# Kernel optimization log

Measured on AMD Instinct MI355X. Metric: run time of the kernel, lower is better.

The kernel has to match this reference:

```python
import jax, jax.numpy as jnp
import numpy as np

N_NODES = 10000
N_EDGES = 320000
N_GRAPHS = 64
L = 3  # num_layers


def _gru(a, h, wih, whh, bih, bhh):
    # torch.nn.GRUCell math: input a, hidden h
    gi = a @ wih.T + bih
    gh = h @ whh.T + bhh
    ir, iz, inn = jnp.split(gi, 3, axis=-1)
    hr, hz, hn = jnp.split(gh, 3, axis=-1)
    r = jax.nn.sigmoid(ir + hr)
    z = jax.nn.sigmoid(iz + hz)
    n = jnp.tanh(inn + r * hn)
    return (1.0 - z) * n + z * h


def _ggc(x, src, dst, w, wih, whh, bih, bhh):
    # PyG GatedGraphConv: pad features up to out_channels, then L rounds of
    # (linear -> scatter-add over edges -> GRUCell update)
    out_ch = w.shape[-1]
    if x.shape[-1] < out_ch:
        x = jnp.concatenate(
            [x, jnp.zeros((x.shape[0], out_ch - x.shape[-1]), x.dtype)], axis=-1)
    for i in range(w.shape[0]):
        m = x @ w[i]                                        # [N, C]
        a = jax.ops.segment_sum(m[src], dst, num_segments=N_NODES)  # scatter-add
        x = _gru(a, x, wih, whh, bih, bhh)
    return x


def setup_inputs() -> dict:
    key = jax.random.key(0)
    ks = jax.random.split(key, 16)
    d1, d2 = 128, 256
    s1, s2 = 1.0 / np.sqrt(d1), 1.0 / np.sqrt(d2)
    x = jax.random.normal(ks[0], (N_NODES, d1), dtype=jnp.float32)
    edge_index = jax.random.randint(ks[1], (2, N_EDGES), 0, N_NODES, dtype=jnp.int64)
    batch = jnp.sort(jax.random.randint(ks[2], (N_NODES,), 0, N_GRAPHS, dtype=jnp.int64))
    return {
        "x": x,
        "edge_index": edge_index,
        "batch": batch,
        "w1": jax.random.normal(ks[3], (L, d1, d1), jnp.float32) * s1,
        "gru1_wih": jax.random.normal(ks[4], (3 * d1, d1), jnp.float32) * s1,
        "gru1_whh": jax.random.normal(ks[5], (3 * d1, d1), jnp.float32) * s1,
        "gru1_bih": jax.random.normal(ks[6], (3 * d1,), jnp.float32) * s1,
        "gru1_bhh": jax.random.normal(ks[7], (3 * d1,), jnp.float32) * s1,
        "w2": jax.random.normal(ks[8], (L, d2, d2), jnp.float32) * s2,
        "gru2_wih": jax.random.normal(ks[9], (3 * d2, d2), jnp.float32) * s2,
        "gru2_whh": jax.random.normal(ks[10], (3 * d2, d2), jnp.float32) * s2,
        "gru2_bih": jax.random.normal(ks[11], (3 * d2,), jnp.float32) * s2,
        "gru2_bhh": jax.random.normal(ks[12], (3 * d2,), jnp.float32) * s2,
        "fc_w": jax.random.normal(ks[13], (6, d2), jnp.float32) * s2,
        "fc_b": jnp.zeros((6,), jnp.float32),
    }


def reference(x, edge_index, batch, w1, gru1_wih, gru1_whh, gru1_bih, gru1_bhh,
              w2, gru2_wih, gru2_whh, gru2_bih, gru2_bhh, fc_w, fc_b):
    src, dst = edge_index[0], edge_index[1]
    y = jax.nn.relu(_ggc(x, src, dst, w1, gru1_wih, gru1_whh, gru1_bih, gru1_bhh))
    y = _ggc(y, src, dst, w2, gru2_wih, gru2_whh, gru2_bih, gru2_bhh)
    y = jax.ops.segment_max(y, batch, num_segments=N_GRAPHS)  # global max pool [G, 256]
    return y @ fc_w.T + fc_b  # [G, 6]
```

## Files before the change

### kernel.cpp

```cpp
#include <hip/hip_runtime.h>

#define NN 10000
#define NNP 10112
#define NE 320000
#define NG 64
#define D1 128
#define D2 256
#define MT 158

typedef unsigned short u16;
typedef short v8s __attribute__((ext_vector_type(8)));
typedef float v4f __attribute__((ext_vector_type(4)));

__device__ __forceinline__ u16 f2bf(float x) {
    unsigned u = __float_as_uint(x);
    return (u16)((u + 0x7fffu + ((u >> 16) & 1u)) >> 16);
}
__device__ __forceinline__ float bf2f(u16 b) {
    return __uint_as_float(((unsigned)b) << 16);
}
__device__ __forceinline__ float sigm(float x) { return 1.f / (1.f + __expf(-x)); }
__device__ __forceinline__ float tanh_f(float x) {
    float cx = fminf(fmaxf(x, -15.f), 15.f);
    float e = __expf(2.f * cx);
    return (e - 1.f) / (e + 1.f);
}

#define MF(d, a, b) d = __builtin_amdgcn_mfma_f32_16x16x32_bf16(a, b, d, 0, 0, 0)

#define SWZ(bx, by)                              \
    const int bid_ = blockIdx.x;                 \
    const int l_ = bid_ >> 3;                    \
    const int by = (bid_ & 7) * 20 + l_ % 20;    \
    const int bx = l_ / 20;                      \
    if (by >= MT) return;


__global__ __launch_bounds__(256)
void mm_k(const u16* __restrict__ Ah, const u16* __restrict__ Al,
          const u16* __restrict__ Bh, const u16* __restrict__ Bl,
          float* __restrict__ Cm, int K) {
    SWZ(bx, by)
    const int tid = threadIdx.x;
    const int wave = tid >> 6, lane = tid & 63;
    const int wm = (wave >> 1) * 32, wn = (wave & 1) * 32;
    const int bm = by * 64, bn = bx * 64;
    const int quad = lane >> 4, r16 = lane & 15;
    const int NK = K >> 5;
    const size_t arow = (size_t)(bm >> 6) * (K >> 3);
    const size_t brow = (size_t)(bn >> 6) * (K >> 3);
    const int aoff0 = (wm + r16) * 8;
    const int boff0 = (wn + r16) * 8;

    auto LOAD = [&](int ks, v8s* af, v8s* alf, v8s* bf, v8s* blf) {
        const size_t ach = (arow + (size_t)(ks << 2) + quad) * 512;
        const size_t bch = (brow + (size_t)(ks << 2) + quad) * 512;
#pragma unroll
        for (int i = 0; i < 2; ++i) {
            af[i]  = *(const v8s*)(Ah + ach + aoff0 + i * 128);
            alf[i] = *(const v8s*)(Al + ach + aoff0 + i * 128);
            bf[i]  = *(const v8s*)(Bh + bch + boff0 + i * 128);
            blf[i] = *(const v8s*)(Bl + bch + boff0 + i * 128);
        }
    };

    v4f acc[2][2] = {};
    auto STEP = [&](v8s* af, v8s* alf, v8s* bf, v8s* blf) {
#pragma unroll
        for (int i = 0; i < 2; ++i)
#pragma unroll
            for (int j = 0; j < 2; ++j) {
                MF(acc[i][j], af[i], bf[j]);
                MF(acc[i][j], af[i], blf[j]);
                MF(acc[i][j], alf[i], bf[j]);
            }
    };

    v8s aA[2], lA[2], bA[2], cA[2];
    v8s aB[2], lB[2], bB[2], cB[2];
    LOAD(0, aA, lA, bA, cA);
    for (int ks = 0; ks < NK; ks += 2) {
        LOAD(ks + 1, aB, lB, bB, cB);
        STEP(aA, lA, bA, cA);
        if (ks + 2 < NK) LOAD(ks + 2, aA, lA, bA, cA);
        STEP(aB, lB, bB, cB);
    }

#pragma unroll
    for (int i = 0; i < 2; ++i) {
        int gr0 = bm + wm + i * 16 + quad * 4;
#pragma unroll
        for (int j = 0; j < 2; ++j) {
            int gc = bn + wn + j * 16 + r16;
#pragma unroll
            for (int r = 0; r < 4; ++r) {
                int gr = gr0 + r;
                if (gr < NN) Cm[(size_t)gr * K + gc] = acc[i][j][r];
            }
        }
    }
}

template<int MODE, int OS>
__global__ __launch_bounds__(256)
void giqru_k(const u16* __restrict__ Ah, const u16* __restrict__ Al,
             const u16* __restrict__ Xh, const u16* __restrict__ Xl,
             const u16* __restrict__ WcH, const u16* __restrict__ WcL,
             const float* __restrict__ bih, const float* __restrict__ bhh,
             u16* __restrict__ xh_out, u16* __restrict__ xl_out,
             const int* __restrict__ batch, unsigned* __restrict__ pool,
             int C) {
    SWZ(bx, by)
    const int tid = threadIdx.x;
    const int wave = tid >> 6, lane = tid & 63;
    const int wm = (wave >> 1) * 32, wn = (wave & 1) * 64;
    const int bm = by * 64, bn = bx * 128;
    const int quad = lane >> 4, r16 = lane & 15;
    const int K2 = 2 * C;
    const int NK = K2 >> 5;
    const int CCH = C >> 3;
    const size_t arow = (size_t)(bm >> 6) * CCH;
    const size_t wrow = (size_t)(bn >> 7) * (K2 >> 3);
    const int aoff0 = (wm + r16) * 8;
    const int woff0 = (wn + r16) * 8;

    auto LOAD = [&](int ks, v8s* fah, v8s* fal, v8s* wh, v8s* wl) {
        const int k0 = ks << 5;
        const bool ap = k0 < C;
        const u16* sh = ap ? Ah : Xh;
        const u16* sl = ap ? Al : Xl;
        const int kk = ap ? k0 : k0 - C;
        const size_t ach = (arow + (kk >> 3) + quad) * 512;
        const size_t wch = (wrow + (k0 >> 3) + quad) * 1024;
        const int g2 = ap ? 2 : 3;
#pragma unroll
        for (int i = 0; i < 2; ++i) {
            fah[i] = *(const v8s*)(sh + ach + aoff0 + i * 128);
            fal[i] = *(const v8s*)(sl + ach + aoff0 + i * 128);
        }
        wh[0] = *(const v8s*)(WcH + wch + woff0);
        wl[0] = *(const v8s*)(WcL + wch + woff0);
        wh[1] = *(const v8s*)(WcH + wch + woff0 + 128);
        wl[1] = *(const v8s*)(WcL + wch + woff0 + 128);
        wh[2] = *(const v8s*)(WcH + wch + woff0 + g2 * 128);
        wl[2] = *(const v8s*)(WcL + wch + woff0 + g2 * 128);
    };

    v4f acc[2][4] = {};
    auto STEP = [&](v8s* fah, v8s* fal, v8s* wh, v8s* wl, bool ap) {
#pragma unroll
        for (int i = 0; i < 2; ++i) {
            MF(acc[i][0], fah[i], wh[0]); MF(acc[i][0], fah[i], wl[0]); MF(acc[i][0], fal[i], wh[0]);
            MF(acc[i][1], fah[i], wh[1]); MF(acc[i][1], fah[i], wl[1]); MF(acc[i][1], fal[i], wh[1]);
            if (ap) {
                MF(acc[i][2], fah[i], wh[2]); MF(acc[i][2], fah[i], wl[2]); MF(acc[i][2], fal[i], wh[2]);
            } else {
                MF(acc[i][3], fah[i], wh[2]); MF(acc[i][3], fah[i], wl[2]); MF(acc[i][3], fal[i], wh[2]);
            }
        }
    };

    v8s ahA[2], alA[2], whA[3], wlA[3];
    v8s ahB[2], alB[2], whB[3], wlB[3];
    LOAD(0, ahA, alA, whA, wlA);
    for (int ks = 0; ks < NK; ks += 2) {
        LOAD(ks + 1, ahB, alB, whB, wlB);
        STEP(ahA, alA, whA, wlA, (ks << 5) < C);
        if (ks + 2 < NK) LOAD(ks + 2, ahA, alA, whA, wlA);
        STEP(ahB, alB, whB, wlB, ((ks + 1) << 5) < C);
    }

    const int c = bx * 32 + (wn ? 16 : 0) + r16;
    const float br = bih[c] + bhh[c];
    const float bz = bih[C + c] + bhh[C + c];
    const float bi_n = bih[2 * C + c];
    const float bh_n = bhh[2 * C + c];
    const int cch = c >> 3, cr = c & 7;
#pragma unroll
    for (int i = 0; i < 2; ++i) {
        int R0 = bm + wm + i * 16 + quad * 4;
#pragma unroll
        for (int r = 0; r < 4; ++r) {
            int R = R0 + r;
            if (R >= NN) continue;
            float rr = sigm(acc[i][0][r] + br);
            float zz = sigm(acc[i][1][r] + bz);
            float nn_ = tanh_f(acc[i][2][r] + bi_n + rr * (acc[i][3][r] + bh_n));
            size_t hx = ((size_t)(R >> 6) * CCH + cch) * 512 + ((R & 63) << 3) + cr;
            float h = bf2f(Xh[hx]) + bf2f(Xl[hx]);
            float o = (1.f - zz) * nn_ + zz * h;
            if (MODE == 2) {
                unsigned b = __float_as_uint(o);
                unsigned u = (b & 0x80000000u) ? ~b : (b | 0x80000000u);
                atomicMax(&pool[batch[R] * 256 + c], u);
            } else {
                if (MODE == 1) o = fmaxf(o, 0.f);
                size_t ox = ((size_t)(R >> 6) * (OS >> 3) + cch) * 512 + ((R & 63) << 3) + cr;
                u16 hh = f2bf(o);
                xh_out[ox] = hh;
                xl_out[ox] = f2bf(o - bf2f(hh));
            }
        }
    }
}

__global__ void count_k(const int* __restrict__ dst, int* __restrict__ cnt) {
    int e = blockIdx.x * blockDim.x + threadIdx.x;
    if (e < NE) atomicAdd(&cnt[dst[e]], 1);
}

__global__ void scan_k(const int* __restrict__ cnt, int* __restrict__ off,
                       int* __restrict__ cur) {
    __shared__ int ps[1024];
    const int tid = threadIdx.x;
    const int CH = (NN + 1023) / 1024;
    const int base = tid * CH;
    int s = 0;
    for (int i = 0; i < CH; ++i) {
        int idx = base + i;
        if (idx < NN) s += cnt[idx];
    }
    ps[tid] = s;
    __syncthreads();
    for (int d = 1; d < 1024; d <<= 1) {
        int v = (tid >= d) ? ps[tid - d] : 0;
        __syncthreads();
        ps[tid] += v;
        __syncthreads();
    }
    int run = (tid > 0) ? ps[tid - 1] : 0;
    for (int i = 0; i < CH; ++i) {
        int idx = base + i;
        if (idx <= NN) { off[idx] = run; if (idx < NN) cur[idx] = run; }
        if (idx < NN) run += cnt[idx];
    }
}

__global__ void fill_k(const int* __restrict__ src, const int* __restrict__ dst,
                       int* __restrict__ cur, int* __restrict__ elist) {
    int e = blockIdx.x * blockDim.x + threadIdx.x;
    if (e >= NE) return;
    int p = atomicAdd(&cur[dst[e]], 1);
    elist[p] = src[e];
}

template<int C>
__global__ void gather_k(const float* __restrict__ m, const int* __restrict__ off,
                         const int* __restrict__ elist,
                         u16* __restrict__ ah, u16* __restrict__ al) {
    constexpr int LPN = C / 4;
    const int GB = gridDim.x;
    const int q = GB >> 3, r = GB & 7;
    const int xx = blockIdx.x & 7, oo = blockIdx.x >> 3;
    const int wg = (xx < r ? xx * (q + 1) : r * (q + 1) + (xx - r) * q) + oo;
    int t = wg * 256 + threadIdx.x;
    int node = t / LPN;
    if (node >= NN) return;
    int c = (t % LPN) * 4;
    int s0 = off[node], s1 = off[node + 1];
    v4f a0 = 0.f, a1 = 0.f, a2 = 0.f, a3 = 0.f;
    int i = s0;
    for (; i + 4 <= s1; i += 4) {
        int e0 = elist[i], e1 = elist[i + 1], e2 = elist[i + 2], e3 = elist[i + 3];
        v4f v0 = *(const v4f*)(m + (size_t)e0 * C + c);
        v4f v1 = *(const v4f*)(m + (size_t)e1 * C + c);
        v4f v2 = *(const v4f*)(m + (size_t)e2 * C + c);
        v4f v3 = *(const v4f*)(m + (size_t)e3 * C + c);
        a0 += v0; a1 += v1; a2 += v2; a3 += v3;
    }
    for (; i < s1; ++i) {
        int e = elist[i];
        a0 += *(const v4f*)(m + (size_t)e * C + c);
    }
    v4f acc = (a0 + a1) + (a2 + a3);
    ushort4 h, l;
    h.x = f2bf(acc[0]); l.x = f2bf(acc[0] - bf2f(h.x));
    h.y = f2bf(acc[1]); l.y = f2bf(acc[1] - bf2f(h.y));
    h.z = f2bf(acc[2]); l.z = f2bf(acc[2] - bf2f(h.z));
    h.w = f2bf(acc[3]); l.w = f2bf(acc[3] - bf2f(h.w));
    size_t ox = ((size_t)(node >> 6) * (C >> 3) + (c >> 3)) * 512 + ((node & 63) << 3) + (c & 7);
    *(ushort4*)(ah + ox) = h;
    *(ushort4*)(al + ox) = l;
}

__global__ void prep_k(const float* __restrict__ w1, const float* __restrict__ w2,
                       const float* __restrict__ wih1, const float* __restrict__ whh1,
                       const float* __restrict__ wih2, const float* __restrict__ whh2,
                       const float* __restrict__ xin,
                       u16* __restrict__ B1h, u16* __restrict__ B1l,
                       u16* __restrict__ B2h, u16* __restrict__ B2l,
                       u16* __restrict__ Wc1h, u16* __restrict__ Wc1l,
                       u16* __restrict__ Wc2h, u16* __restrict__ Wc2l,
                       u16* __restrict__ xh, u16* __restrict__ xl) {
    const int n1 = 3 * D1 * D1;
    const int n2 = 3 * D2 * D2;
    const int c1 = 4 * D1 * 2 * D1;
    const int c2 = 4 * D2 * 2 * D2;
    int t = blockIdx.x * blockDim.x + threadIdx.x;
    if (t < n1) {
        int l = t / (D1 * D1), rem = t - l * (D1 * D1);
        int k = rem / D1, n = rem - k * D1;
        float v = w1[t]; u16 h = f2bf(v);
        size_t o = l * D1 * D1 + ((size_t)(n >> 6) * (D1 >> 3) + (k >> 3)) * 512 + ((n & 63) << 3) + (k & 7);
        B1h[o] = h; B1l[o] = f2bf(v - bf2f(h)); return;
    }
    t -= n1;
    if (t < n2) {
        int l = t / (D2 * D2), rem = t - l * (D2 * D2);
        int k = rem / D2, n = rem - k * D2;
        float v = w2[t]; u16 h = f2bf(v);
        size_t o = l * D2 * D2 + ((size_t)(n >> 6) * (D2 >> 3) + (k >> 3)) * 512 + ((n & 63) << 3) + (k & 7);
        B2h[o] = h; B2l[o] = f2bf(v - bf2f(h)); return;
    }
    t -= n2;
    if (t < c1) {
        int jp = t >> 8, k = t & 255;
        int c = ((jp >> 6) << 4) | (jp & 15);
        int g = (jp >> 4) & 3;
        float v;
        if (g == 0)      v = (k < D1) ? wih1[c * D1 + k]            : whh1[c * D1 + k - D1];
        else if (g == 1) v = (k < D1) ? wih1[(D1 + c) * D1 + k]     : whh1[(D1 + c) * D1 + k - D1];
        else if (g == 2) v = (k < D1) ? wih1[(2 * D1 + c) * D1 + k] : 0.f;
        else             v = (k < D1) ? 0.f : whh1[(2 * D1 + c) * D1 + k - D1];
        u16 h = f2bf(v);
        size_t o = ((size_t)(jp >> 7) * 32 + (k >> 3)) * 1024 + ((jp & 127) << 3) + (k & 7);
        Wc1h[o] = h; Wc1l[o] = f2bf(v - bf2f(h)); return;
    }
    t -= c1;
    if (t < c2) {
        int jp = t >> 9, k = t & 511;
        int c = ((jp >> 6) << 4) | (jp & 15);
        int g = (jp >> 4) & 3;
        float v;
        if (g == 0)      v = (k < D2) ? wih2[c * D2 + k]            : whh2[c * D2 + k - D2];
        else if (g == 1) v = (k < D2) ? wih2[(D2 + c) * D2 + k]     : whh2[(D2 + c) * D2 + k - D2];
        else if (g == 2) v = (k < D2) ? wih2[(2 * D2 + c) * D2 + k] : 0.f;
        else             v = (k < D2) ? 0.f : whh2[(2 * D2 + c) * D2 + k - D2];
        u16 h = f2bf(v);
        size_t o = ((size_t)(jp >> 7) * 64 + (k >> 3)) * 1024 + ((jp & 127) << 3) + (k & 7);
        Wc2h[o] = h; Wc2l[o] = f2bf(v - bf2f(h)); return;
    }
    t -= c2;
    if (t < NN * D1) {
        int n = t >> 7, cc = t & 127;
        float v = xin[t];
        u16 h = f2bf(v);
        size_t o = ((size_t)(n >> 6) * 16 + (cc >> 3)) * 512 + ((n & 63) << 3) + (cc & 7);
        xh[o] = h;
        xl[o] = f2bf(v - bf2f(h));
    }
}

__global__ void pad_k(u16* __restrict__ xh, u16* __restrict__ xl) {
    int t = blockIdx.x * blockDim.x + threadIdx.x;
    if (t >= NNP * 128) return;
    int n = t >> 7, c = 128 + (t & 127);
    size_t o = ((size_t)(n >> 6) * 32 + (c >> 3)) * 512 + ((n & 63) << 3) + (c & 7);
    xh[o] = 0;
    xl[o] = 0;
}

__global__ void pool_init_k(unsigned* __restrict__ pool) {
    int t = blockIdx.x * blockDim.x + threadIdx.x;
    if (t < NG * D2) pool[t] = 0x007FFFFFu;
}

__global__ void fc_k(const unsigned* __restrict__ pool, const float* __restrict__ w,
                     const float* __restrict__ b, float* __restrict__ out) {
    int t = blockIdx.x * blockDim.x + threadIdx.x;
    if (t >= NG * 6) return;
    int g = t / 6, o = t - g * 6;
    float s = b[o];
    for (int c = 0; c < D2; ++c) {
        unsigned u = pool[g * D2 + c];
        unsigned bits = (u & 0x80000000u) ? (u ^ 0x80000000u) : ~u;
        s += __uint_as_float(bits) * w[o * D2 + c];
    }
    out[t] = s;
}

extern "C" void kernel_launch(void* const* d_in, const int* in_sizes, int n_in,
                              void* d_out, int out_size, void* d_ws, size_t ws_size,
                              hipStream_t stream) {
    const float* x_in = (const float*)d_in[0];
    const int* ei = (const int*)d_in[1];
    const int* src = ei;
    const int* dst = ei + NE;
    const int* batch = (const int*)d_in[2];
    const float* w1   = (const float*)d_in[3];
    const float* wih1 = (const float*)d_in[4];
    const float* whh1 = (const float*)d_in[5];
    const float* bih1 = (const float*)d_in[6];
    const float* bhh1 = (const float*)d_in[7];
    const float* w2   = (const float*)d_in[8];
    const float* wih2 = (const float*)d_in[9];
    const float* whh2 = (const float*)d_in[10];
    const float* bih2 = (const float*)d_in[11];
    const float* bhh2 = (const float*)d_in[12];
    const float* fcw  = (const float*)d_in[13];
    const float* fcb  = (const float*)d_in[14];
    float* out = (float*)d_out;

    float* ws = (float*)d_ws;
    float* mbuf = ws;
    u16* a_h  = (u16*)(mbuf + (size_t)NNP * 256);
    u16* a_l  = a_h + (size_t)NNP * 256;
    u16* xA0h = a_l + (size_t)NNP * 256;
    u16* xA0l = xA0h + (size_t)NNP * 128;
    u16* xA1h = xA0l + (size_t)NNP * 128;
    u16* xA1l = xA1h + (size_t)NNP * 128;
    u16* xB0h = xA1l + (size_t)NNP * 128;
    u16* xB0l = xB0h + (size_t)NNP * 256;
    u16* xB1h = xB0l + (size_t)NNP * 256;
    u16* xB1l = xB1h + (size_t)NNP * 256;
    u16* B1h  = xB1l + (size_t)NNP * 256;
    u16* B1l  = B1h + 3 * D1 * D1;
    u16* B2h  = B1l + 3 * D1 * D1;
    u16* B2l  = B2h + 3 * D2 * D2;
    u16* Wc1h = B2l + 3 * D2 * D2;
    u16* Wc1l = Wc1h + 4 * D1 * 2 * D1;
    u16* Wc2h = Wc1l + 4 * D1 * 2 * D1;
    u16* Wc2l = Wc2h + 4 * D2 * 2 * D2;
    int* cnt   = (int*)(Wc2l + 4 * D2 * 2 * D2);
    int* off   = cnt + NN;
    int* cur   = off + NN + 1;
    int* elist = cur + NN;
    unsigned* pool = (unsigned*)(elist + NE);

    hipMemsetAsync(cnt, 0, NN * sizeof(int), stream);
    count_k<<<(NE + 255) / 256, 256, 0, stream>>>(dst, cnt);
    scan_k<<<1, 1024, 0, stream>>>(cnt, off, cur);
    fill_k<<<(NE + 255) / 256, 256, 0, stream>>>(src, dst, cur, elist);
    {
        int total = 3 * D1 * D1 + 3 * D2 * D2 + 4 * D1 * 2 * D1 + 4 * D2 * 2 * D2 + NN * D1;
        prep_k<<<(total + 255) / 256, 256, 0, stream>>>(
            w1, w2, wih1, whh1, wih2, whh2, x_in,
            B1h, B1l, B2h, B2l, Wc1h, Wc1l, Wc2h, Wc2l, xA0h, xA0l);
    }
    pad_k<<<(NNP * 128 + 255) / 256, 256, 0, stream>>>(xB0h, xB0l);
    pool_init_k<<<(NG * D2 + 255) / 256, 256, 0, stream>>>(pool);

    const int M1 = 160 * (D1 / 64);
    const int M2 = 160 * (D2 / 64);
    const int G1 = 160 * (D1 / 32);
    const int G2 = 160 * (D2 / 32);
    const int GG1 = (NN * (D1 / 4) + 255) / 256;
    const int GG2 = (NN * (D2 / 4) + 255) / 256;

    mm_k<<<M1, 256, 0, stream>>>(xA0h, xA0l, B1h, B1l, mbuf, D1);
    gather_k<D1><<<GG1, 256, 0, stream>>>(mbuf, off, elist, a_h, a_l);
    giqru_k<0, 128><<<G1, 256, 0, stream>>>(
        a_h, a_l, xA0h, xA0l, Wc1h, Wc1l, bih1, bhh1,
        xA1h, xA1l, nullptr, nullptr, D1);

    mm_k<<<M1, 256, 0, stream>>>(xA1h, xA1l, B1h + D1 * D1, B1l + D1 * D1, mbuf, D1);
    gather_k<D1><<<GG1, 256, 0, stream>>>(mbuf, off, elist, a_h, a_l);
    giqru_k<0, 128><<<G1, 256, 0, stream>>>(
        a_h, a_l, xA1h, xA1l, Wc1h, Wc1l, bih1, bhh1,
        xA0h, xA0l, nullptr, nullptr, D1);

    mm_k<<<M1, 256, 0, stream>>>(xA0h, xA0l, B1h + 2 * D1 * D1, B1l + 2 * D1 * D1, mbuf, D1);
    gather_k<D1><<<GG1, 256, 0, stream>>>(mbuf, off, elist, a_h, a_l);
    giqru_k<1, 256><<<G1, 256, 0, stream>>>(
        a_h, a_l, xA0h, xA0l, Wc1h, Wc1l, bih1, bhh1,
        xB0h, xB0l, nullptr, nullptr, D1);

    mm_k<<<M2, 256, 0, stream>>>(xB0h, xB0l, B2h, B2l, mbuf, D2);
    gather_k<D2><<<GG2, 256, 0, stream>>>(mbuf, off, elist, a_h, a_l);
    giqru_k<0, 256><<<G2, 256, 0, stream>>>(
        a_h, a_l, xB0h, xB0l, Wc2h, Wc2l, bih2, bhh2,
        xB1h, xB1l, nullptr, nullptr, D2);

    mm_k<<<M2, 256, 0, stream>>>(xB1h, xB1l, B2h + D2 * D2, B2l + D2 * D2, mbuf, D2);
    gather_k<D2><<<GG2, 256, 0, stream>>>(mbuf, off, elist, a_h, a_l);
    giqru_k<0, 256><<<G2, 256, 0, stream>>>(
        a_h, a_l, xB1h, xB1l, Wc2h, Wc2l, bih2, bhh2,
        xB0h, xB0l, nullptr, nullptr, D2);

    mm_k<<<M2, 256, 0, stream>>>(xB0h, xB0l, B2h + 2 * D2 * D2, B2l + 2 * D2 * D2, mbuf, D2);
    gather_k<D2><<<GG2, 256, 0, stream>>>(mbuf, off, elist, a_h, a_l);
    giqru_k<2, 256><<<G2, 256, 0, stream>>>(
        a_h, a_l, xB0h, xB0l, Wc2h, Wc2l, bih2, bhh2,
        nullptr, nullptr, batch, pool, D2);

    fc_k<<<1, 512, 0, stream>>>(pool, fcw, fcb, out);
}
```

Before: 557.6 us.

## Fold per-layer linear into GRU input weights and gather raw features

```diff
diff --git a/kernel.cpp b/kernel.cpp
--- a/kernel.cpp
+++ b/kernel.cpp
@@ -36,78 +36,14 @@
     if (by >= MT) return;
 
 
-__global__ __launch_bounds__(256)
-void mm_k(const u16* __restrict__ Ah, const u16* __restrict__ Al,
-          const u16* __restrict__ Bh, const u16* __restrict__ Bl,
-          float* __restrict__ Cm, int K) {
-    SWZ(bx, by)
-    const int tid = threadIdx.x;
-    const int wave = tid >> 6, lane = tid & 63;
-    const int wm = (wave >> 1) * 32, wn = (wave & 1) * 32;
-    const int bm = by * 64, bn = bx * 64;
-    const int quad = lane >> 4, r16 = lane & 15;
-    const int NK = K >> 5;
-    const size_t arow = (size_t)(bm >> 6) * (K >> 3);
-    const size_t brow = (size_t)(bn >> 6) * (K >> 3);
-    const int aoff0 = (wm + r16) * 8;
-    const int boff0 = (wn + r16) * 8;
-
-    auto LOAD = [&](int ks, v8s* af, v8s* alf, v8s* bf, v8s* blf) {
-        const size_t ach = (arow + (size_t)(ks << 2) + quad) * 512;
-        const size_t bch = (brow + (size_t)(ks << 2) + quad) * 512;
-#pragma unroll
-        for (int i = 0; i < 2; ++i) {
-            af[i]  = *(const v8s*)(Ah + ach + aoff0 + i * 128);
-            alf[i] = *(const v8s*)(Al + ach + aoff0 + i * 128);
-            bf[i]  = *(const v8s*)(Bh + bch + boff0 + i * 128);
-            blf[i] = *(const v8s*)(Bl + bch + boff0 + i * 128);
-        }
-    };
-
-    v4f acc[2][2] = {};
-    auto STEP = [&](v8s* af, v8s* alf, v8s* bf, v8s* blf) {
-#pragma unroll
-        for (int i = 0; i < 2; ++i)
-#pragma unroll
-            for (int j = 0; j < 2; ++j) {
-                MF(acc[i][j], af[i], bf[j]);
-                MF(acc[i][j], af[i], blf[j]);
-                MF(acc[i][j], alf[i], bf[j]);
-            }
-    };
-
-    v8s aA[2], lA[2], bA[2], cA[2];
-    v8s aB[2], lB[2], bB[2], cB[2];
-    LOAD(0, aA, lA, bA, cA);
-    for (int ks = 0; ks < NK; ks += 2) {
-        LOAD(ks + 1, aB, lB, bB, cB);
-        STEP(aA, lA, bA, cA);
-        if (ks + 2 < NK) LOAD(ks + 2, aA, lA, bA, cA);
-        STEP(aB, lB, bB, cB);
-    }
-
-#pragma unroll
-    for (int i = 0; i < 2; ++i) {
-        int gr0 = bm + wm + i * 16 + quad * 4;
-#pragma unroll
-        for (int j = 0; j < 2; ++j) {
-            int gc = bn + wn + j * 16 + r16;
-#pragma unroll
-            for (int r = 0; r < 4; ++r) {
-                int gr = gr0 + r;
-                if (gr < NN) Cm[(size_t)gr * K + gc] = acc[i][j][r];
-            }
-        }
-    }
-}
-
 template<int MODE, int OS>
-__global__ __launch_bounds__(256)
+__global__ __launch_bounds__(256, 3)
 void giqru_k(const u16* __restrict__ Ah, const u16* __restrict__ Al,
              const u16* __restrict__ Xh, const u16* __restrict__ Xl,
              const u16* __restrict__ WcH, const u16* __restrict__ WcL,
              const float* __restrict__ bih, const float* __restrict__ bhh,
              u16* __restrict__ xh_out, u16* __restrict__ xl_out,
+             float* __restrict__ xf_out,
              const int* __restrict__ batch, unsigned* __restrict__ pool,
              int C) {
     SWZ(bx, by)
@@ -199,6 +135,7 @@
                 u16 hh = f2bf(o);
                 xh_out[ox] = hh;
                 xl_out[ox] = f2bf(o - bf2f(hh));
+                xf_out[(size_t)R * OS + c] = o;
             }
         }
     }
@@ -245,7 +182,7 @@
 }
 
 template<int C>
-__global__ void gather_k(const float* __restrict__ m, const int* __restrict__ off,
+__global__ void gather_k(const float* __restrict__ xf, const int* __restrict__ off,
                          const int* __restrict__ elist,
                          u16* __restrict__ ah, u16* __restrict__ al) {
     constexpr int LPN = C / 4;
@@ -262,15 +199,15 @@
     int i = s0;
     for (; i + 4 <= s1; i += 4) {
         int e0 = elist[i], e1 = elist[i + 1], e2 = elist[i + 2], e3 = elist[i + 3];
-        v4f v0 = *(const v4f*)(m + (size_t)e0 * C + c);
-        v4f v1 = *(const v4f*)(m + (size_t)e1 * C + c);
-        v4f v2 = *(const v4f*)(m + (size_t)e2 * C + c);
-        v4f v3 = *(const v4f*)(m + (size_t)e3 * C + c);
+        v4f v0 = *(const v4f*)(xf + (size_t)e0 * C + c);
+        v4f v1 = *(const v4f*)(xf + (size_t)e1 * C + c);
+        v4f v2 = *(const v4f*)(xf + (size_t)e2 * C + c);
+        v4f v3 = *(const v4f*)(xf + (size_t)e3 * C + c);
         a0 += v0; a1 += v1; a2 += v2; a3 += v3;
     }
     for (; i < s1; ++i) {
         int e = elist[i];
-        a0 += *(const v4f*)(m + (size_t)e * C + c);
+        a0 += *(const v4f*)(xf + (size_t)e * C + c);
     }
     v4f acc = (a0 + a1) + (a2 + a3);
     ushort4 h, l;
@@ -283,64 +220,95 @@
     *(ushort4*)(al + ox) = l;
 }
 
-__global__ void prep_k(const float* __restrict__ w1, const float* __restrict__ w2,
-                       const float* __restrict__ wih1, const float* __restrict__ whh1,
-                       const float* __restrict__ wih2, const float* __restrict__ whh2,
+__global__ void weff_k(const float* __restrict__ w, const float* __restrict__ wih,
+                       u16* __restrict__ WcH, u16* __restrict__ WcL, int C) {
+    __shared__ float As[64 * 65];
+    __shared__ float Bs[64 * 65];
+    const int k0 = blockIdx.x * 64, jp0 = blockIdx.y * 64, it = blockIdx.z;
+    const int tid = threadIdx.x;
+    const int tx = tid & 15, ty = tid >> 4;
+    const int K2 = 2 * C;
+    float acc[4][4] = {};
+    for (int j0 = 0; j0 < C; j0 += 64) {
+        for (int idx = tid; idx < 4096; idx += 256) {
+            int row = idx >> 6, j = idx & 63;
+            As[row * 65 + j] = w[((size_t)it * C + k0 + row) * C + j0 + j];
+            int jp = jp0 + row;
+            int cc = ((jp >> 6) << 4) | (jp & 15);
+            int g = (jp >> 4) & 3;
+            Bs[row * 65 + j] = (g < 3) ? wih[((size_t)g * C + cc) * C + j0 + j] : 0.f;
+        }
+        __syncthreads();
+        for (int j = 0; j < 64; ++j) {
+            float a0 = As[(tx * 4 + 0) * 65 + j];
+            float a1 = As[(tx * 4 + 1) * 65 + j];
+            float a2 = As[(tx * 4 + 2) * 65 + j];
+            float a3 = As[(tx * 4 + 3) * 65 + j];
+            float b0 = Bs[(ty * 4 + 0) * 65 + j];
+            float b1 = Bs[(ty * 4 + 1) * 65 + j];
+            float b2 = Bs[(ty * 4 + 2) * 65 + j];
+            float b3 = Bs[(ty * 4 + 3) * 65 + j];
+            acc[0][0] += b0 * a0; acc[0][1] += b0 * a1; acc[0][2] += b0 * a2; acc[0][3] += b0 * a3;
+            acc[1][0] += b1 * a0; acc[1][1] += b1 * a1; acc[1][2] += b1 * a2; acc[1][3] += b1 * a3;
+            acc[2][0] += b2 * a0; acc[2][1] += b2 * a1; acc[2][2] += b2 * a2; acc[2][3] += b2 * a3;
+            acc[3][0] += b3 * a0; acc[3][1] += b3 * a1; acc[3][2] += b3 * a2; acc[3][3] += b3 * a3;
+        }
+        __syncthreads();
+    }
+    const size_t its = (size_t)it * 8 * C * C;
+#pragma unroll
+    for (int a = 0; a < 4; ++a) {
+        int jp = jp0 + ty * 4 + a;
+#pragma unroll
+        for (int b = 0; b < 4; ++b) {
+            int k = k0 + tx * 4 + b;
+            float v = acc[a][b];
+            u16 h = f2bf(v);
+            size_t o = its + ((size_t)(jp >> 7) * (K2 >> 3) + (k >> 3)) * 1024 + ((jp & 127) << 3) + (k & 7);
+            WcH[o] = h;
+            WcL[o] = f2bf(v - bf2f(h));
+        }
+    }
+}
+
+__global__ void prep_k(const float* __restrict__ whh1, const float* __restrict__ whh2,
                        const float* __restrict__ xin,
-                       u16* __restrict__ B1h, u16* __restrict__ B1l,
-                       u16* __restrict__ B2h, u16* __restrict__ B2l,
                        u16* __restrict__ Wc1h, u16* __restrict__ Wc1l,
                        u16* __restrict__ Wc2h, u16* __restrict__ Wc2l,
                        u16* __restrict__ xh, u16* __restrict__ xl) {
-    const int n1 = 3 * D1 * D1;
-    const int n2 = 3 * D2 * D2;
-    const int c1 = 4 * D1 * 2 * D1;
-    const int c2 = 4 * D2 * 2 * D2;
+    const int q1 = 3 * 512 * 128;
+    const int q2 = 3 * 1024 * 256;
     int t = blockIdx.x * blockDim.x + threadIdx.x;
-    if (t < n1) {
-        int l = t / (D1 * D1), rem = t - l * (D1 * D1);
-        int k = rem / D1, n = rem - k * D1;
-        float v = w1[t]; u16 h = f2bf(v);
-        size_t o = l * D1 * D1 + ((size_t)(n >> 6) * (D1 >> 3) + (k >> 3)) * 512 + ((n & 63) << 3) + (k & 7);
-        B1h[o] = h; B1l[o] = f2bf(v - bf2f(h)); return;
-    }
-    t -= n1;
-    if (t < n2) {
-        int l = t / (D2 * D2), rem = t - l * (D2 * D2);
-        int k = rem / D2, n = rem - k * D2;
-        float v = w2[t]; u16 h = f2bf(v);
-        size_t o = l * D2 * D2 + ((size_t)(n >> 6) * (D2 >> 3) + (k >> 3)) * 512 + ((n & 63) << 3) + (k & 7);
-        B2h[o] = h; B2l[o] = f2bf(v - bf2f(h)); return;
-    }
-    t -= n2;
-    if (t < c1) {
-        int jp = t >> 8, k = t & 255;
+    if (t < q1) {
+        int it = t / (512 * 128), r = t - it * (512 * 128);
+        int jp = r >> 7, kk = r & 127;
         int c = ((jp >> 6) << 4) | (jp & 15);
         int g = (jp >> 4) & 3;
-        float v;
-        if (g == 0)      v = (k < D1) ? wih1[c * D1 + k]            : whh1[c * D1 + k - D1];
-        else if (g == 1) v = (k < D1) ? wih1[(D1 + c) * D1 + k]     : whh1[(D1 + c) * D1 + k - D1];
-        else if (g == 2) v = (k < D1) ? wih1[(2 * D1 + c) * D1 + k] : 0.f;
-        else             v = (k < D1) ? 0.f : whh1[(2 * D1 + c) * D1 + k - D1];
+        float v = (g == 0) ? whh1[c * D1 + kk]
+                : (g == 1) ? whh1[(D1 + c) * D1 + kk]
+                : (g == 2) ? 0.f
+                           : whh1[(2 * D1 + c) * D1 + kk];
+        int k = D1 + kk;
         u16 h = f2bf(v);
-        size_t o = ((size_t)(jp >> 7) * 32 + (k >> 3)) * 1024 + ((jp & 127) << 3) + (k & 7);
+        size_t o = (size_t)it * 131072 + ((size_t)(jp >> 7) * 32 + (k >> 3)) * 1024 + ((jp & 127) << 3) + (k & 7);
         Wc1h[o] = h; Wc1l[o] = f2bf(v - bf2f(h)); return;
     }
-    t -= c1;
-    if (t < c2) {
-        int jp = t >> 9, k = t & 511;
+    t -= q1;
+    if (t < q2) {
+        int it = t / (1024 * 256), r = t - it * (1024 * 256);
+        int jp = r >> 8, kk = r & 255;
         int c = ((jp >> 6) << 4) | (jp & 15);
         int g = (jp >> 4) & 3;
-        float v;
-        if (g == 0)      v = (k < D2) ? wih2[c * D2 + k]            : whh2[c * D2 + k - D2];
-        else if (g == 1) v = (k < D2) ? wih2[(D2 + c) * D2 + k]     : whh2[(D2 + c) * D2 + k - D2];
-        else if (g == 2) v = (k < D2) ? wih2[(2 * D2 + c) * D2 + k] : 0.f;
-        else             v = (k < D2) ? 0.f : whh2[(2 * D2 + c) * D2 + k - D2];
+        float v = (g == 0) ? whh2[c * D2 + kk]
+                : (g == 1) ? whh2[(D2 + c) * D2 + kk]
+                : (g == 2) ? 0.f
+                           : whh2[(2 * D2 + c) * D2 + kk];
+        int k = D2 + kk;
         u16 h = f2bf(v);
-        size_t o = ((size_t)(jp >> 7) * 64 + (k >> 3)) * 1024 + ((jp & 127) << 3) + (k & 7);
+        size_t o = (size_t)it * 524288 + ((size_t)(jp >> 7) * 64 + (k >> 3)) * 1024 + ((jp & 127) << 3) + (k & 7);
         Wc2h[o] = h; Wc2l[o] = f2bf(v - bf2f(h)); return;
     }
-    t -= c2;
+    t -= q2;
     if (t < NN * D1) {
         int n = t >> 7, cc = t & 127;
         float v = xin[t];
@@ -351,13 +319,15 @@
     }
 }
 
-__global__ void pad_k(u16* __restrict__ xh, u16* __restrict__ xl) {
+__global__ void pad_k(u16* __restrict__ xh, u16* __restrict__ xl,
+                      float* __restrict__ xf) {
     int t = blockIdx.x * blockDim.x + threadIdx.x;
     if (t >= NNP * 128) return;
     int n = t >> 7, c = 128 + (t & 127);
     size_t o = ((size_t)(n >> 6) * 32 + (c >> 3)) * 512 + ((n & 63) << 3) + (c & 7);
     xh[o] = 0;
     xl[o] = 0;
+    xf[(size_t)n * 256 + c] = 0.f;
 }
 
 __global__ void pool_init_k(unsigned* __restrict__ pool) {
@@ -401,9 +371,7 @@
     const float* fcb  = (const float*)d_in[14];
     float* out = (float*)d_out;
 
-    float* ws = (float*)d_ws;
-    float* mbuf = ws;
-    u16* a_h  = (u16*)(mbuf + (size_t)NNP * 256);
+    u16* a_h  = (u16*)d_ws;
     u16* a_l  = a_h + (size_t)NNP * 256;
     u16* xA0h = a_l + (size_t)NNP * 256;
     u16* xA0l = xA0h + (size_t)NNP * 128;
@@ -413,15 +381,13 @@
     u16* xB0l = xB0h + (size_t)NNP * 256;
     u16* xB1h = xB0l + (size_t)NNP * 256;
     u16* xB1l = xB1h + (size_t)NNP * 256;
-    u16* B1h  = xB1l + (size_t)NNP * 256;
-    u16* B1l  = B1h + 3 * D1 * D1;
-    u16* B2h  = B1l + 3 * D1 * D1;
-    u16* B2l  = B2h + 3 * D2 * D2;
-    u16* Wc1h = B2l + 3 * D2 * D2;
-    u16* Wc1l = Wc1h + 4 * D1 * 2 * D1;
-    u16* Wc2h = Wc1l + 4 * D1 * 2 * D1;
-    u16* Wc2l = Wc2h + 4 * D2 * 2 * D2;
-    int* cnt   = (int*)(Wc2l + 4 * D2 * 2 * D2);
+    u16* Wc1h = xB1l + (size_t)NNP * 256;
+    u16* Wc1l = Wc1h + (size_t)3 * 512 * 256;
+    u16* Wc2h = Wc1l + (size_t)3 * 512 * 256;
+    u16* Wc2l = Wc2h + (size_t)3 * 1024 * 512;
+    float* xfA = (float*)(Wc2l + (size_t)3 * 1024 * 512);
+    float* xfB = xfA + (size_t)NNP * 128;
+    int* cnt   = (int*)(xfB + (size_t)NNP * 256);
     int* off   = cnt + NN;
     int* cur   = off + NN + 1;
     int* elist = cur + NN;
@@ -432,56 +398,50 @@
     scan_k<<<1, 1024, 0, stream>>>(cnt, off, cur);
     fill_k<<<(NE + 255) / 256, 256, 0, stream>>>(src, dst, cur, elist);
     {
-        int total = 3 * D1 * D1 + 3 * D2 * D2 + 4 * D1 * 2 * D1 + 4 * D2 * 2 * D2 + NN * D1;
+        int total = 3 * 512 * 128 + 3 * 1024 * 256 + NN * D1;
         prep_k<<<(total + 255) / 256, 256, 0, stream>>>(
-            w1, w2, wih1, whh1, wih2, whh2, x_in,
-            B1h, B1l, B2h, B2l, Wc1h, Wc1l, Wc2h, Wc2l, xA0h, xA0l);
-    }
-    pad_k<<<(NNP * 128 + 255) / 256, 256, 0, stream>>>(xB0h, xB0l);
+            whh1, whh2, x_in, Wc1h, Wc1l, Wc2h, Wc2l, xA0h, xA0l);
+    }
+    weff_k<<<dim3(D1 / 64, 4 * D1 / 64, 3), 256, 0, stream>>>(w1, wih1, Wc1h, Wc1l, D1);
+    weff_k<<<dim3(D2 / 64, 4 * D2 / 64, 3), 256, 0, stream>>>(w2, wih2, Wc2h, Wc2l, D2);
+    pad_k<<<(NNP * 128 + 255) / 256, 256, 0, stream>>>(xB0h, xB0l, xfB);
     pool_init_k<<<(NG * D2 + 255) / 256, 256, 0, stream>>>(pool);
 
-    const int M1 = 160 * (D1 / 64);
-    const int M2 = 160 * (D2 / 64);
-    const int G1 = 160 * (D1 / 32);
-    const int G2 = 160 * (D2 / 32);
+    const int G1 = 160 * 4;
+    const int G2 = 160 * 8;
     const int GG1 = (NN * (D1 / 4) + 255) / 256;
     const int GG2 = (NN * (D2 / 4) + 255) / 256;
-
-    mm_k<<<M1, 256, 0, stream>>>(xA0h, xA0l, B1h, B1l, mbuf, D1);
-    gather_k<D1><<<GG1, 256, 0, stream>>>(mbuf, off, elist, a_h, a_l);
+    const size_t W1S = 131072, W2S = 524288;
+
+    gather_k<D1><<<GG1, 256, 0, stream>>>(x_in, off, elist, a_h, a_l);
     giqru_k<0, 128><<<G1, 256, 0, stream>>>(
         a_h, a_l, xA0h, xA0l, Wc1h, Wc1l, bih1, bhh1,
-        xA1h, xA1l, nullptr, nullptr, D1);
-
-    mm_k<<<M1, 256, 0, stream>>>(xA1h, xA1l, B1h + D1 * D1, B1l + D1 * D1, mbuf, D1);
-    gather_k<D1><<<GG1, 256, 0, stream>>>(mbuf, off, elist, a_h, a_l);
+        xA1h, xA1l, xfA, nullptr, nullptr, D1);
+
+    gather_k<D1><<<GG1, 256, 0, stream>>>(xfA, off, elist, a_h, a_l);
     giqru_k<0, 128><<<G1, 256, 0, stream>>>(
-        a_h, a_l, xA1h, xA1l, Wc1h, Wc1l, bih1, bhh1,
-        xA0h, xA0l, nullptr, nullptr, D1);
-
-    mm_k<<<M1, 256, 0, stream>>>(xA0h, xA0l, B1h + 2 * D1 * D1, B1l + 2 * D1 * D1, mbuf, D1);
-    gather_k<D1><<<GG1, 256, 0, stream>>>(mbuf, off, elist, a_h, a_l);
+        a_h, a_l, xA1h, xA1l, Wc1h + W1S, Wc1l + W1S, bih1, bhh1,
+        xA0h, xA0l, xfA, nullptr, nullptr, D1);
+
+    gather_k<D1><<<GG1, 256, 0, stream>>>(xfA, off, elist, a_h, a_l);
     giqru_k<1, 256><<<G1, 256, 0, stream>>>(
-        a_h, a_l, xA0h, xA0l, Wc1h, Wc1l, bih1, bhh1,
-        xB0h, xB0l, nullptr, nullptr, D1);
-
-    mm_k<<<M2, 256, 0, stream>>>(xB0h, xB0l, B2h, B2l, mbuf, D2);
-    gather_k<D2><<<GG2, 256, 0, stream>>>(mbuf, off, elist, a_h, a_l);
+        a_h, a_l, xA0h, xA0l, Wc1h + 2 * W1S, Wc1l + 2 * W1S, bih1, bhh1,
+        xB0h, xB0l, xfB, nullptr, nullptr, D1);
+
+    gather_k<D2><<<GG2, 256, 0, stream>>>(xfB, off, elist, a_h, a_l);
     giqru_k<0, 256><<<G2, 256, 0, stream>>>(
         a_h, a_l, xB0h, xB0l, Wc2h, Wc2l, bih2, bhh2,
-        xB1h, xB1l, nullptr, nullptr, D2);
-
-    mm_k<<<M2, 256, 0, stream>>>(xB1h, xB1l, B2h + D2 * D2, B2l + D2 * D2, mbuf, D2);
-    gather_k<D2><<<GG2, 256, 0, stream>>>(mbuf, off, elist, a_h, a_l);
+        xB1h, xB1l, xfB, nullptr, nullptr, D2);
+
+    gather_k<D2><<<GG2, 256, 0, stream>>>(xfB, off, elist, a_h, a_l);
     giqru_k<0, 256><<<G2, 256, 0, stream>>>(
-        a_h, a_l, xB1h, xB1l, Wc2h, Wc2l, bih2, bhh2,
-        xB0h, xB0l, nullptr, nullptr, D2);
-
-    mm_k<<<M2, 256, 0, stream>>>(xB0h, xB0l, B2h + 2 * D2 * D2, B2l + 2 * D2 * D2, mbuf, D2);
-    gather_k<D2><<<GG2, 256, 0, stream>>>(mbuf, off, elist, a_h, a_l);
+        a_h, a_l, xB1h, xB1l, Wc2h + W2S, Wc2l + W2S, bih2, bhh2,
+        xB0h, xB0l, xfB, nullptr, nullptr, D2);
+
+    gather_k<D2><<<GG2, 256, 0, stream>>>(xfB, off, elist, a_h, a_l);
     giqru_k<2, 256><<<G2, 256, 0, stream>>>(
-        a_h, a_l, xB0h, xB0l, Wc2h, Wc2l, bih2, bhh2,
-        nullptr, nullptr, batch, pool, D2);
+        a_h, a_l, xB0h, xB0l, Wc2h + 2 * W2S, Wc2l + 2 * W2S, bih2, bhh2,
+        nullptr, nullptr, nullptr, batch, pool, D2);
 
     fc_k<<<1, 512, 0, stream>>>(pool, fcw, fcb, out);
 }
```

After: 576.7 us. +3.4%, slower.
